# Optimization experiments

Hardware: AMD Instinct MI355X
Metric: run time of the kernel (lower is better)

## Reference

```python
import jax, jax.numpy as jnp
import numpy as np

B, S, E, H, WIN = 2, 4096, 768, 12, 256
D = E // H


def layer_norm(x, g, b, eps=1e-5):
    m = jnp.mean(x, axis=-1, keepdims=True)
    v = jnp.mean((x - m) ** 2, axis=-1, keepdims=True)
    return (x - m) * jax.lax.rsqrt(v + eps) * g + b


def sliding_window_attention(q, k, v, w):
    """Exact symmetric banded attention (Longformer sliding_chunks): each query
    attends to keys in [i-w, i+w], edges masked to -inf (autoregressive=False).
    q,k,v: (B,H,S,D). Returns (B,H,S,D)."""
    b, h, s, d = q.shape
    nb = s // w  # number of query blocks of width w
    q = q * (1.0 / jnp.sqrt(jnp.asarray(d, q.dtype)))
    qb = q.reshape(b, h, nb, w, d)

    def blocks3(t):
        # overlapping key/value blocks of length 3w with stride w (zero halo pad)
        tp = jnp.pad(t, ((0, 0), (0, 0), (w, w), (0, 0)))
        tw = tp.reshape(b, h, nb + 2, w, d)
        return jnp.concatenate([tw[:, :, 0:nb], tw[:, :, 1:nb + 1], tw[:, :, 2:nb + 2]], axis=3)  # (B,H,nb,3w,D)

    kb = blocks3(k)
    vb = blocks3(v)

    # (B,H,nb,w,3w): query block c local x vs key window local y (global j = c*w - w + y)
    scores = jnp.einsum('bhcxd,bhcyd->bhcxy', qb, kb)

    x_idx = jnp.arange(w)[:, None]            # (w,1) local query pos
    y_idx = jnp.arange(3 * w)[None, :]        # (1,3w) local key pos
    diag_ok = (y_idx >= x_idx) & (y_idx <= x_idx + 2 * w)   # |j - i| <= w
    c_idx = jnp.arange(nb)[:, None, None]     # (nb,1,1)
    j = c_idx * w - w + y_idx[None]           # (nb,1,3w) global key index
    in_seq = (j >= 0) & (j < s)
    mask = diag_ok[None] & in_seq             # (nb,w,3w)

    neg = jnp.finfo(scores.dtype).min
    scores = jnp.where(mask[None, None], scores, neg)
    p = jax.nn.softmax(scores, axis=-1)
    out = jnp.einsum('bhcxy,bhcyd->bhcxd', p, vb)
    return out.reshape(b, h, s, d)


def setup_inputs() -> dict:
    key = jax.random.key(0)
    ks = jax.random.split(key, 6)
    std = 0.02
    return {
        'x': jax.random.normal(ks[0], (B, S, E), jnp.float32),
        'ln1_g': jnp.ones((E,), jnp.float32),
        'ln1_b': jnp.zeros((E,), jnp.float32),
        'c_attn_w': jax.random.normal(ks[1], (E, 3 * E), jnp.float32) * std,
        'c_attn_b': jnp.zeros((3 * E,), jnp.float32),
        'c_proj_w': jax.random.normal(ks[2], (E, E), jnp.float32) * std,
        'c_proj_b': jnp.zeros((E,), jnp.float32),
        'ln2_g': jnp.ones((E,), jnp.float32),
        'ln2_b': jnp.zeros((E,), jnp.float32),
        'fc_w': jax.random.normal(ks[3], (E, 4 * E), jnp.float32) * std,
        'fc_b': jnp.zeros((4 * E,), jnp.float32),
        'proj2_w': jax.random.normal(ks[4], (4 * E, E), jnp.float32) * std,
        'proj2_b': jnp.zeros((E,), jnp.float32),
        'w': WIN,
    }


def reference(x, ln1_g, ln1_b, c_attn_w, c_attn_b, c_proj_w, c_proj_b,
              ln2_g, ln2_b, fc_w, fc_b, proj2_w, proj2_b, w):
    b, s, e = x.shape
    h = layer_norm(x, ln1_g, ln1_b)
    qkv = h @ c_attn_w + c_attn_b                 # (B,S,3E)
    q, k, v = jnp.split(qkv, 3, axis=-1)
    q = q.reshape(b, s, H, D).transpose(0, 2, 1, 3)
    k = k.reshape(b, s, H, D).transpose(0, 2, 1, 3)
    v = v.reshape(b, s, H, D).transpose(0, 2, 1, 3)
    a = sliding_window_attention(q, k, v, int(w))  # (B,H,S,D)
    a = a.transpose(0, 2, 1, 3).reshape(b, s, e)
    x = x + a @ c_proj_w + c_proj_b
    h2 = layer_norm(x, ln2_g, ln2_b)
    ff = jax.nn.gelu(h2 @ fc_w + fc_b, approximate=False)
    x = x + ff @ proj2_w + proj2_b
    return x
```

## Files before the change

### kernel.cpp

```cpp
#include <hip/hip_runtime.h>
#include <cstdint>
#include <cstddef>

typedef unsigned short US;
typedef __attribute__((ext_vector_type(8))) short bf16x8_t;
typedef __attribute__((ext_vector_type(4))) float f32x4_t;
typedef __attribute__((ext_vector_type(4))) int   i32x4_t;
typedef __attribute__((ext_vector_type(2))) unsigned int u32x2_t;

__device__ __forceinline__ float bf2f(US u) {
  union { unsigned int i; float f; } c; c.i = ((unsigned int)u) << 16; return c.f;
}
__device__ __forceinline__ US f2bf(float f) {
  union { float f; unsigned int i; } c; c.f = f;
  unsigned int i = c.i;
  return (US)((i + 0x7fffu + ((i >> 16) & 1u)) >> 16);
}

__device__ __forceinline__ void async16(const US* g, US* l) {
  __builtin_amdgcn_global_load_lds((const __attribute__((address_space(1))) void*)g,
                                   (__attribute__((address_space(3))) void*)l,
                                   16, 0, 0);
}

__global__ __launch_bounds__(256) void ln_kernel(const float* __restrict__ x,
                                                 const float* __restrict__ g,
                                                 const float* __restrict__ b,
                                                 US* __restrict__ out) {
  int wv = threadIdx.x >> 6, lane = threadIdx.x & 63;
  long row = (long)blockIdx.x * 4 + wv;
  const float* xr = x + row * 768 + lane * 12;
  f32x4_t d0 = *(const f32x4_t*)(xr);
  f32x4_t d1 = *(const f32x4_t*)(xr + 4);
  f32x4_t d2 = *(const f32x4_t*)(xr + 8);
  float v[12] = {d0[0], d0[1], d0[2], d0[3], d1[0], d1[1], d1[2], d1[3],
                 d2[0], d2[1], d2[2], d2[3]};
  float s = 0.f, sq = 0.f;
  for (int k = 0; k < 12; k++) { s += v[k]; sq += v[k]*v[k]; }
  for (int m = 1; m < 64; m <<= 1) { s += __shfl_xor(s, m, 64); sq += __shfl_xor(sq, m, 64); }
  float mean = s * (1.f/768.f);
  float var  = sq * (1.f/768.f) - mean*mean;
  float rs   = rsqrtf(var + 1e-5f);
  const float* gp = g + lane*12;
  const float* bp = b + lane*12;
  unsigned int o[6];
  for (int k = 0; k < 6; k++) {
    US r0 = f2bf((v[2*k]   - mean) * rs * gp[2*k]   + bp[2*k]);
    US r1 = f2bf((v[2*k+1] - mean) * rs * gp[2*k+1] + bp[2*k+1]);
    o[k] = (unsigned int)r0 | ((unsigned int)r1 << 16);
  }
  US* orow = out + row * 768 + lane * 12;
  *(u32x2_t*)(orow)     = (u32x2_t){o[0], o[1]};
  *(u32x2_t*)(orow + 4) = (u32x2_t){o[2], o[3]};
  *(u32x2_t*)(orow + 8) = (u32x2_t){o[4], o[5]};
}

__global__ __launch_bounds__(256) void cvtT_kernel(const float* __restrict__ in,
                                                   US* __restrict__ out,
                                                   int K, int N) {
  __shared__ float tile[32][33];
  int bx = blockIdx.x * 32;
  int by = blockIdx.y * 32;
  int tx = threadIdx.x, ty = threadIdx.y;
  for (int i = ty; i < 32; i += 8) tile[i][tx] = in[(long)(by + i) * N + bx + tx];
  __syncthreads();
  for (int i = ty; i < 32; i += 8) out[(long)(bx + i) * K + by + tx] = f2bf(tile[tx][i]);
}

template <int EPI, int OUTBF>
__global__ __launch_bounds__(256) void gemm_bt(const US* __restrict__ A,
                                               const US* __restrict__ Bt,
                                               const float* __restrict__ bias,
                                               const float* __restrict__ res,
                                               void* __restrict__ Cv,
                                               int M, int N, int K) {
  __shared__ US As[128 * 32];
  __shared__ US Bs[128 * 32];
  const int tid  = threadIdx.x;
  const int lane = tid & 63;
  const int wv   = tid >> 6;
  const int quad = lane >> 4;
  const int l15  = lane & 15;
  const int wm   = (wv >> 1) * 64;
  const int wn   = (wv & 1) * 64;
  const long bm  = (long)blockIdx.x * 128;
  const long bn  = (long)blockIdx.y * 128;

  const int srow  = wv * 16 + (lane >> 2);
  const int skoff = (lane & 3) * 8;
  const US* Ag  = A  + (bm + srow) * (long)K + skoff;
  const US* Ag2 = Ag + 64 * (long)K;
  const US* Bg  = Bt + (bn + srow) * (long)K + skoff;
  const US* Bg2 = Bg + 64 * (long)K;
  US* Asl  = As + wv * 512;
  US* Asl2 = As + 2048 + wv * 512;
  US* Bsl  = Bs + wv * 512;
  US* Bsl2 = Bs + 2048 + wv * 512;

  f32x4_t acc[4][4] = {};

  for (int k0 = 0; k0 < K; k0 += 32) {
    __syncthreads();
    async16(Ag  + k0, Asl);
    async16(Ag2 + k0, Asl2);
    async16(Bg  + k0, Bsl);
    async16(Bg2 + k0, Bsl2);
    __syncthreads();
    bf16x8_t af[4], bfr[4];
    for (int t = 0; t < 4; t++)
      af[t]  = *(const bf16x8_t*)(As + (wm + t*16 + l15) * 32 + quad * 8);
    for (int t = 0; t < 4; t++)
      bfr[t] = *(const bf16x8_t*)(Bs + (wn + t*16 + l15) * 32 + quad * 8);
    for (int r = 0; r < 4; r++)
      for (int c = 0; c < 4; c++)
        acc[r][c] = __builtin_amdgcn_mfma_f32_16x16x32_bf16(af[r], bfr[c], acc[r][c], 0, 0, 0);
  }

  US*    Cb = (US*)Cv;
  float* Cf = (float*)Cv;
  for (int c = 0; c < 4; c++) {
    long gcol = bn + wn + c*16 + l15;
    float bv = bias[gcol];
    for (int r = 0; r < 4; r++) {
      long grow0 = bm + wm + r*16 + quad*4;
      for (int i = 0; i < 4; i++) {
        long idx = (grow0 + i) * (long)N + gcol;
        float v = acc[r][c][i] + bv;
        if (EPI == 1) v += res[idx];
        if (EPI == 2) v = 0.5f * v * (1.0f + erff(v * 0.70710678118654752f));
        if (OUTBF) Cb[idx] = f2bf(v);
        else       Cf[idx] = v;
      }
    }
  }
}

template <int EPI, int OUTBF>
__global__ __launch_bounds__(256) void gemm_kn(const US* __restrict__ A,
                                               const float* __restrict__ B,
                                               const float* __restrict__ bias,
                                               const float* __restrict__ res,
                                               void* __restrict__ Cv,
                                               int M, int N, int K) {
  __shared__ US As[128 * 48];
  __shared__ US Bs[128 * 48];
  const int tid  = threadIdx.x;
  const int lane = tid & 63;
  const int wv   = tid >> 6;
  const int quad = lane >> 4;
  const int l15  = lane & 15;
  const int wm   = (wv >> 1) * 64;
  const int wn   = (wv & 1) * 64;
  const long bm  = (long)blockIdx.x * 128;
  const long bn  = (long)blockIdx.y * 128;

  const int srow = tid >> 1;
  const int scol = (tid & 1) * 16;
  const US* Ag = A + (bm + srow) * (long)K + scol;
  US* Asw = As + srow * 48 + scol;
  const float* Bg = B + bn + lane;

  f32x4_t acc[4][4] = {};

  for (int k0 = 0; k0 < K; k0 += 32) {
    i32x4_t a0 = *(const i32x4_t*)(Ag + k0);
    i32x4_t a1 = *(const i32x4_t*)(Ag + k0 + 8);
    unsigned int bv0[4], bv1[4];
    for (int kp = 0; kp < 4; kp++) {
      long rof = (long)(k0 + wv * 8 + kp * 2) * N;
      US lo0 = f2bf(Bg[rof]);
      US hi0 = f2bf(Bg[rof + N]);
      US lo1 = f2bf(Bg[rof + 64]);
      US hi1 = f2bf(Bg[rof + N + 64]);
      bv0[kp] = (unsigned int)lo0 | ((unsigned int)hi0 << 16);
      bv1[kp] = (unsigned int)lo1 | ((unsigned int)hi1 << 16);
    }
    __syncthreads();
    *(i32x4_t*)(Asw)     = a0;
    *(i32x4_t*)(Asw + 8) = a1;
    for (int kp = 0; kp < 4; kp++) {
      *(unsigned int*)(Bs + lane * 48 + wv * 8 + kp * 2)        = bv0[kp];
      *(unsigned int*)(Bs + (64 + lane) * 48 + wv * 8 + kp * 2) = bv1[kp];
    }
    __syncthreads();
    bf16x8_t af[4], bfr[4];
    for (int t = 0; t < 4; t++)
      af[t]  = *(const bf16x8_t*)(As + (wm + t*16 + l15) * 48 + quad * 8);
    for (int t = 0; t < 4; t++)
      bfr[t] = *(const bf16x8_t*)(Bs + (wn + t*16 + l15) * 48 + quad * 8);
    for (int r = 0; r < 4; r++)
      for (int c = 0; c < 4; c++)
        acc[r][c] = __builtin_amdgcn_mfma_f32_16x16x32_bf16(af[r], bfr[c], acc[r][c], 0, 0, 0);
  }

  US*    Cb = (US*)Cv;
  float* Cf = (float*)Cv;
  for (int c = 0; c < 4; c++) {
    long gcol = bn + wn + c*16 + l15;
    float bv = bias[gcol];
    for (int r = 0; r < 4; r++) {
      long grow0 = bm + wm + r*16 + quad*4;
      for (int i = 0; i < 4; i++) {
        long idx = (grow0 + i) * (long)N + gcol;
        float v = acc[r][c][i] + bv;
        if (EPI == 1) v += res[idx];
        if (EPI == 2) v = 0.5f * v * (1.0f + erff(v * 0.70710678118654752f));
        if (OUTBF) Cb[idx] = f2bf(v);
        else       Cf[idx] = v;
      }
    }
  }
}

__global__ __launch_bounds__(256) void attn_kernel(const US* __restrict__ qkv,
                                                   US* __restrict__ aout) {
  __shared__ US Qs [64 * 72];
  __shared__ US Ks [64 * 72];
  __shared__ US Vts[64 * 72];
  __shared__ US Ps [4 * 16 * 72];

  const int tid  = threadIdx.x;
  const int lane = tid & 63;
  const int wv   = tid >> 6;
  const int quad = lane >> 4;
  const int l15  = lane & 15;

  const int qt = blockIdx.x & 63;
  const int hh = (blockIdx.x >> 6) % 12;
  const int bb = blockIdx.x / (64 * 12);
  const int q0 = qt * 64;
  const long tokbase = (long)bb * 4096;
  const int qoff = hh * 64;
  const int koff = 768 + qoff;
  const int voff = 1536 + qoff;

  for (int it = 0; it < 2; it++) {
    int idx = tid + it * 256;
    int r = idx >> 3, part = (idx & 7) * 8;
    i32x4_t d = *(const i32x4_t*)(qkv + (tokbase + q0 + r) * 2304 + qoff + part);
    *(i32x4_t*)(Qs + r * 72 + part) = d;
  }

  f32x4_t O[4] = {};
  float mst[4] = {-INFINITY, -INFINITY, -INFINITY, -INFINITY};
  float lst[4] = {0.f, 0.f, 0.f, 0.f};
  const float sc2 = 0.125f * 1.4426950408889634f;

  for (int t = 0; t < 9; t++) {
    const int kt0 = q0 - 256 + t * 64;
    if (kt0 + 63 < 0 || kt0 >= 4096) continue;
    __syncthreads();
    for (int it = 0; it < 2; it++) {
      int idx = tid + it * 256;
      int r = idx >> 3, part = (idx & 7) * 8;
      int kg = kt0 + r;
      i32x4_t d = {};
      if (kg >= 0 && kg < 4096)
        d = *(const i32x4_t*)(qkv + (tokbase + kg) * 2304 + koff + part);
      *(i32x4_t*)(Ks + r * 72 + part) = d;
    }
    for (int it = 0; it < 2; it++) {
      int idx = tid + it * 256;
      int dd = idx >> 3, kg8 = (idx & 7) * 8;
      alignas(16) US tmp[8];
      for (int l = 0; l < 8; l++) {
        int kg = kt0 + kg8 + l;
        tmp[l] = (kg >= 0 && kg < 4096) ? qkv[(tokbase + kg) * 2304 + voff + dd] : (US)0;
      }
      *(i32x4_t*)(Vts + dd * 72 + kg8) = *(const i32x4_t*)tmp;
    }
    __syncthreads();

    bf16x8_t aq0 = *(const bf16x8_t*)(Qs + (wv*16 + l15) * 72 + quad * 8);
    bf16x8_t aq1 = *(const bf16x8_t*)(Qs + (wv*16 + l15) * 72 + 32 + quad * 8);
    float p[4][4];
    float mtile[4] = {-INFINITY, -INFINITY, -INFINITY, -INFINITY};
    const int qrow0 = q0 + wv*16 + quad*4;
    for (int c = 0; c < 4; c++) {
      bf16x8_t bk0 = *(const bf16x8_t*)(Ks + (c*16 + l15) * 72 + quad * 8);
      bf16x8_t bk1 = *(const bf16x8_t*)(Ks + (c*16 + l15) * 72 + 32 + quad * 8);
      f32x4_t z = {};
      z = __builtin_amdgcn_mfma_f32_16x16x32_bf16(aq0, bk0, z, 0, 0, 0);
      z = __builtin_amdgcn_mfma_f32_16x16x32_bf16(aq1, bk1, z, 0, 0, 0);
      int kglob = kt0 + c*16 + l15;
      bool kin = (kglob >= 0) && (kglob < 4096);
      for (int i = 0; i < 4; i++) {
        int qg = qrow0 + i;
        bool ok = kin && (kglob >= qg - 256) && (kglob <= qg + 256);
        p[c][i] = ok ? z[i] * sc2 : -INFINITY;
        mtile[i] = fmaxf(mtile[i], p[c][i]);
      }
    }
    for (int m = 1; m < 16; m <<= 1)
      for (int i = 0; i < 4; i++) mtile[i] = fmaxf(mtile[i], __shfl_xor(mtile[i], m, 64));
    float alpha[4];
    for (int i = 0; i < 4; i++) {
      float mn = fmaxf(mst[i], mtile[i]);
      alpha[i] = (mst[i] > -INFINITY) ? exp2f(mst[i] - mn) : 0.f;
      mst[i] = mn;
    }
    float rsum[4] = {0.f, 0.f, 0.f, 0.f};
    for (int c = 0; c < 4; c++)
      for (int i = 0; i < 4; i++) {
        float pv = (mst[i] > -INFINITY && p[c][i] > -INFINITY) ? exp2f(p[c][i] - mst[i]) : 0.f;
        p[c][i] = pv;
        rsum[i] += pv;
      }
    for (int m = 1; m < 16; m <<= 1)
      for (int i = 0; i < 4; i++) rsum[i] += __shfl_xor(rsum[i], m, 64);
    for (int i = 0; i < 4; i++) lst[i] = lst[i] * alpha[i] + rsum[i];
    for (int c2 = 0; c2 < 4; c2++)
      for (int i = 0; i < 4; i++) O[c2][i] *= alpha[i];
    for (int c = 0; c < 4; c++)
      for (int i = 0; i < 4; i++)
        Ps[wv*1152 + (quad*4 + i) * 72 + c*16 + l15] = f2bf(p[c][i]);
    bf16x8_t ap0 = *(const bf16x8_t*)(Ps + wv*1152 + l15 * 72 + quad * 8);
    bf16x8_t ap1 = *(const bf16x8_t*)(Ps + wv*1152 + l15 * 72 + 32 + quad * 8);
    for (int c2 = 0; c2 < 4; c2++) {
      bf16x8_t bv0 = *(const bf16x8_t*)(Vts + (c2*16 + l15) * 72 + quad * 8);
      bf16x8_t bv1 = *(const bf16x8_t*)(Vts + (c2*16 + l15) * 72 + 32 + quad * 8);
      O[c2] = __builtin_amdgcn_mfma_f32_16x16x32_bf16(ap0, bv0, O[c2], 0, 0, 0);
      O[c2] = __builtin_amdgcn_mfma_f32_16x16x32_bf16(ap1, bv1, O[c2], 0, 0, 0);
    }
  }

  for (int c2 = 0; c2 < 4; c2++)
    for (int i = 0; i < 4; i++) {
      long tok = tokbase + q0 + wv*16 + quad*4 + i;
      float ov = O[c2][i] / lst[i];
      aout[tok * 768 + qoff + c2*16 + l15] = f2bf(ov);
    }
}

extern "C" void kernel_launch(void* const* d_in, const int* in_sizes, int n_in,
                              void* d_out, int out_size, void* d_ws, size_t ws_size,
                              hipStream_t stream) {
  const float* x        = (const float*)d_in[0];
  const float* ln1_g    = (const float*)d_in[1];
  const float* ln1_b    = (const float*)d_in[2];
  const float* c_attn_w = (const float*)d_in[3];
  const float* c_attn_b = (const float*)d_in[4];
  const float* c_proj_w = (const float*)d_in[5];
  const float* c_proj_b = (const float*)d_in[6];
  const float* ln2_g    = (const float*)d_in[7];
  const float* ln2_b    = (const float*)d_in[8];
  const float* fc_w     = (const float*)d_in[9];
  const float* fc_b     = (const float*)d_in[10];
  const float* proj2_w  = (const float*)d_in[11];
  const float* proj2_b  = (const float*)d_in[12];

  US*    hba = (US*)d_ws;
  US*    qkv = hba + 8192L * 768;
  US*    ff  = qkv;
  float* x1  = (float*)d_out;
  float* out = (float*)d_out;

  const size_t FAST_NEED = 77070336;
  if (ws_size >= FAST_NEED) {
    US* wqkvT = (US*)((char*)d_ws + 62914560);
    US* wprjT = wqkvT + 2304L * 768;
    US* wfcT  = wprjT + 768L * 768;
    US* wp2T  = wfcT  + 3072L * 768;
    dim3 tb(32, 8);
    cvtT_kernel<<<dim3(2304/32,  768/32), tb, 0, stream>>>(c_attn_w, wqkvT, 768, 2304);
    cvtT_kernel<<<dim3( 768/32,  768/32), tb, 0, stream>>>(c_proj_w, wprjT, 768,  768);
    cvtT_kernel<<<dim3(3072/32,  768/32), tb, 0, stream>>>(fc_w,     wfcT,  768, 3072);
    cvtT_kernel<<<dim3( 768/32, 3072/32), tb, 0, stream>>>(proj2_w,  wp2T, 3072,  768);

    ln_kernel<<<2048, 256, 0, stream>>>(x, ln1_g, ln1_b, hba);
    gemm_bt<0,1><<<dim3(64, 18), 256, 0, stream>>>(hba, wqkvT, c_attn_b, nullptr,
                                                   qkv, 8192, 2304, 768);
    attn_kernel<<<1536, 256, 0, stream>>>(qkv, hba);
    gemm_bt<1,0><<<dim3(64, 6), 256, 0, stream>>>(hba, wprjT, c_proj_b, x,
                                                  x1, 8192, 768, 768);
    ln_kernel<<<2048, 256, 0, stream>>>(x1, ln2_g, ln2_b, hba);
    gemm_bt<2,1><<<dim3(64, 24), 256, 0, stream>>>(hba, wfcT, fc_b, nullptr,
                                                   ff, 8192, 3072, 768);
    gemm_bt<1,0><<<dim3(64, 6), 256, 0, stream>>>(ff, wp2T, proj2_b, x1,
                                                  out, 8192, 768, 3072);
  } else {
    ln_kernel<<<2048, 256, 0, stream>>>(x, ln1_g, ln1_b, hba);
    gemm_kn<0,1><<<dim3(64, 18), 256, 0, stream>>>(hba, c_attn_w, c_attn_b, nullptr,
                                                   qkv, 8192, 2304, 768);
    attn_kernel<<<1536, 256, 0, stream>>>(qkv, hba);
    gemm_kn<1,0><<<dim3(64, 6), 256, 0, stream>>>(hba, c_proj_w, c_proj_b, x,
                                                  x1, 8192, 768, 768);
    ln_kernel<<<2048, 256, 0, stream>>>(x1, ln2_g, ln2_b, hba);
    gemm_kn<2,1><<<dim3(64, 24), 256, 0, stream>>>(hba, fc_w, fc_b, nullptr,
                                                   ff, 8192, 3072, 768);
    gemm_kn<1,0><<<dim3(64, 6), 256, 0, stream>>>(ff, proj2_w, proj2_b, x1,
                                                  out, 8192, 768, 3072);
  }
}
```

Measured before the change: 448.8 us.

## Double K-step in bf16 GEMM, polynomial GELU, vectorized V loads in attention

```diff
diff --git a/kernel.cpp b/kernel.cpp
--- a/kernel.cpp
+++ b/kernel.cpp
@@ -21,6 +21,16 @@
   __builtin_amdgcn_global_load_lds((const __attribute__((address_space(1))) void*)g,
                                    (__attribute__((address_space(3))) void*)l,
                                    16, 0, 0);
+}
+
+__device__ __forceinline__ float gelu_exact(float v) {
+  float y = fabsf(v) * 0.70710678118654752f;
+  float t = 1.0f / (1.0f + 0.3275911f * y);
+  float poly = ((((1.061405429f * t - 1.453152027f) * t + 1.421413741f) * t
+                 - 0.284496736f) * t + 0.254829592f) * t;
+  float erfv = 1.0f - poly * __expf(-y * y);
+  erfv = copysignf(erfv, v);
+  return 0.5f * v * (1.0f + erfv);
 }
 
 __global__ __launch_bounds__(256) void ln_kernel(const float* __restrict__ x,
@@ -74,8 +84,10 @@
                                                const float* __restrict__ res,
                                                void* __restrict__ Cv,
                                                int M, int N, int K) {
-  __shared__ US As[128 * 32];
-  __shared__ US Bs[128 * 32];
+  __shared__ US As0[128 * 32];
+  __shared__ US As1[128 * 32];
+  __shared__ US Bs0[128 * 32];
+  __shared__ US Bs1[128 * 32];
   const int tid  = threadIdx.x;
   const int lane = tid & 63;
   const int wv   = tid >> 6;
@@ -92,28 +104,44 @@
   const US* Ag2 = Ag + 64 * (long)K;
   const US* Bg  = Bt + (bn + srow) * (long)K + skoff;
   const US* Bg2 = Bg + 64 * (long)K;
-  US* Asl  = As + wv * 512;
-  US* Asl2 = As + 2048 + wv * 512;
-  US* Bsl  = Bs + wv * 512;
-  US* Bsl2 = Bs + 2048 + wv * 512;
+  US* a0l  = As0 + wv * 512;   US* a0l2 = As0 + 2048 + wv * 512;
+  US* a1l  = As1 + wv * 512;   US* a1l2 = As1 + 2048 + wv * 512;
+  US* b0l  = Bs0 + wv * 512;   US* b0l2 = Bs0 + 2048 + wv * 512;
+  US* b1l  = Bs1 + wv * 512;   US* b1l2 = Bs1 + 2048 + wv * 512;
 
   f32x4_t acc[4][4] = {};
 
-  for (int k0 = 0; k0 < K; k0 += 32) {
-    __syncthreads();
-    async16(Ag  + k0, Asl);
-    async16(Ag2 + k0, Asl2);
-    async16(Bg  + k0, Bsl);
-    async16(Bg2 + k0, Bsl2);
-    __syncthreads();
-    bf16x8_t af[4], bfr[4];
-    for (int t = 0; t < 4; t++)
-      af[t]  = *(const bf16x8_t*)(As + (wm + t*16 + l15) * 32 + quad * 8);
-    for (int t = 0; t < 4; t++)
-      bfr[t] = *(const bf16x8_t*)(Bs + (wn + t*16 + l15) * 32 + quad * 8);
-    for (int r = 0; r < 4; r++)
-      for (int c = 0; c < 4; c++)
-        acc[r][c] = __builtin_amdgcn_mfma_f32_16x16x32_bf16(af[r], bfr[c], acc[r][c], 0, 0, 0);
+  for (int k0 = 0; k0 < K; k0 += 64) {
+    __syncthreads();
+    async16(Ag  + k0,      a0l);
+    async16(Ag2 + k0,      a0l2);
+    async16(Ag  + k0 + 32, a1l);
+    async16(Ag2 + k0 + 32, a1l2);
+    async16(Bg  + k0,      b0l);
+    async16(Bg2 + k0,      b0l2);
+    async16(Bg  + k0 + 32, b1l);
+    async16(Bg2 + k0 + 32, b1l2);
+    __syncthreads();
+    {
+      bf16x8_t af[4], bfr[4];
+      for (int t = 0; t < 4; t++)
+        af[t]  = *(const bf16x8_t*)(As0 + (wm + t*16 + l15) * 32 + quad * 8);
+      for (int t = 0; t < 4; t++)
+        bfr[t] = *(const bf16x8_t*)(Bs0 + (wn + t*16 + l15) * 32 + quad * 8);
+      for (int r = 0; r < 4; r++)
+        for (int c = 0; c < 4; c++)
+          acc[r][c] = __builtin_amdgcn_mfma_f32_16x16x32_bf16(af[r], bfr[c], acc[r][c], 0, 0, 0);
+    }
+    {
+      bf16x8_t af[4], bfr[4];
+      for (int t = 0; t < 4; t++)
+        af[t]  = *(const bf16x8_t*)(As1 + (wm + t*16 + l15) * 32 + quad * 8);
+      for (int t = 0; t < 4; t++)
+        bfr[t] = *(const bf16x8_t*)(Bs1 + (wn + t*16 + l15) * 32 + quad * 8);
+      for (int r = 0; r < 4; r++)
+        for (int c = 0; c < 4; c++)
+          acc[r][c] = __builtin_amdgcn_mfma_f32_16x16x32_bf16(af[r], bfr[c], acc[r][c], 0, 0, 0);
+    }
   }
 
   US*    Cb = (US*)Cv;
@@ -127,7 +155,7 @@
         long idx = (grow0 + i) * (long)N + gcol;
         float v = acc[r][c][i] + bv;
         if (EPI == 1) v += res[idx];
-        if (EPI == 2) v = 0.5f * v * (1.0f + erff(v * 0.70710678118654752f));
+        if (EPI == 2) v = gelu_exact(v);
         if (OUTBF) Cb[idx] = f2bf(v);
         else       Cf[idx] = v;
       }
@@ -204,7 +232,7 @@
         long idx = (grow0 + i) * (long)N + gcol;
         float v = acc[r][c][i] + bv;
         if (EPI == 1) v += res[idx];
-        if (EPI == 2) v = 0.5f * v * (1.0f + erff(v * 0.70710678118654752f));
+        if (EPI == 2) v = gelu_exact(v);
         if (OUTBF) Cb[idx] = f2bf(v);
         else       Cf[idx] = v;
       }
@@ -254,20 +282,18 @@
       int idx = tid + it * 256;
       int r = idx >> 3, part = (idx & 7) * 8;
       int kg = kt0 + r;
-      i32x4_t d = {};
-      if (kg >= 0 && kg < 4096)
-        d = *(const i32x4_t*)(qkv + (tokbase + kg) * 2304 + koff + part);
-      *(i32x4_t*)(Ks + r * 72 + part) = d;
-    }
-    for (int it = 0; it < 2; it++) {
-      int idx = tid + it * 256;
-      int dd = idx >> 3, kg8 = (idx & 7) * 8;
+      bool in = (kg >= 0 && kg < 4096);
+      i32x4_t dk = {}, dv = {};
+      if (in) {
+        const US* base = qkv + (tokbase + kg) * 2304;
+        dk = *(const i32x4_t*)(base + koff + part);
+        dv = *(const i32x4_t*)(base + voff + part);
+      }
+      *(i32x4_t*)(Ks + r * 72 + part) = dk;
       alignas(16) US tmp[8];
-      for (int l = 0; l < 8; l++) {
-        int kg = kt0 + kg8 + l;
-        tmp[l] = (kg >= 0 && kg < 4096) ? qkv[(tokbase + kg) * 2304 + voff + dd] : (US)0;
-      }
-      *(i32x4_t*)(Vts + dd * 72 + kg8) = *(const i32x4_t*)tmp;
+      *(i32x4_t*)tmp = dv;
+      for (int j = 0; j < 8; j++)
+        Vts[(part + j) * 72 + r] = tmp[j];
     }
     __syncthreads();
 
```

New measurement: 426.6 us. 1.05x faster.
